# Performance work log

Hardware: AMD Instinct MI355X
Metric: run time of the kernel (lower is better)

Reference implementation:

```python
import jax, jax.numpy as jnp
import numpy as np

B = 8
N_PER = 8192   # xyz points per batch
M_PER = 2048   # query points per batch
C_FEAT = 32
RADIUS = 0.2
K = 32         # sample_nums
USE_XYZ = True


def setup_inputs() -> dict:
    key = jax.random.key(0)
    k1, k2, k3 = jax.random.split(key, 3)
    xyz = jax.random.uniform(k1, (B * N_PER, 3), dtype=jnp.float32)
    new_xyz = jax.random.uniform(k2, (B * M_PER, 3), dtype=jnp.float32)
    features = jax.random.normal(k3, (B * N_PER, C_FEAT), dtype=jnp.float32)
    xyz_batch_cnt = jnp.full((B,), N_PER, dtype=jnp.int32)
    new_xyz_batch_cnt = jnp.full((B,), M_PER, dtype=jnp.int32)
    return {
        "xyz": xyz,
        "xyz_batch_cnt": xyz_batch_cnt,
        "new_xyz": new_xyz,
        "new_xyz_batch_cnt": new_xyz_batch_cnt,
        "features": features,
    }


def _ball_query(xyz_b, new_b, radius, k):
    # xyz_b: (B, N, 3), new_b: (B, M, 3)
    n = xyz_b.shape[1]
    # squared pairwise distances (B, M, N)
    d2 = jnp.sum((new_b[:, :, None, :] - xyz_b[:, None, :, :]) ** 2, axis=-1)
    mask = d2 < (radius * radius)
    # first-k in-radius indices (CUDA ball_query keeps neighbors in point order)
    scores = jnp.where(mask, jnp.arange(n, dtype=jnp.int32), jnp.int32(n))
    idx_sorted = jnp.sort(scores, axis=-1)[..., :k]          # (B, M, k)
    cnt = jnp.sum(mask, axis=-1)                              # (B, M)
    empty = cnt == 0                                          # (B, M)
    first = idx_sorted[..., :1]                               # duplicate first hit
    slot = jnp.arange(k, dtype=jnp.int32)
    idx = jnp.where(slot[None, None, :] < cnt[..., None], idx_sorted, first)
    idx = jnp.where(empty[..., None], jnp.int32(0), idx)      # empty balls -> 0
    return idx, empty


def reference(xyz, xyz_batch_cnt, new_xyz, new_xyz_batch_cnt, features):
    b = xyz_batch_cnt.shape[0]
    xyz_b = xyz.reshape(b, -1, 3)          # (B, N, 3)
    new_b = new_xyz.reshape(b, -1, 3)      # (B, M, 3)
    feat_b = features.reshape(b, xyz_b.shape[1], -1)  # (B, N, C)

    idx, empty = _ball_query(xyz_b, new_b, RADIUS, K)  # (B, M, K), (B, M)

    gather = jax.vmap(lambda pts, i: pts[i])           # per-batch gather
    grouped_xyz = gather(xyz_b, idx) - new_b[:, :, None, :]   # (B, M, K, 3)
    grouped_xyz = jnp.where(empty[..., None, None], 0.0, grouped_xyz)

    grouped_feat = gather(feat_b, idx)                        # (B, M, K, C)
    grouped_feat = jnp.where(empty[..., None, None], 0.0, grouped_feat)

    if USE_XYZ:
        new_features = jnp.concatenate([grouped_xyz, grouped_feat], axis=-1)
    else:
        new_features = grouped_feat
    # (B, M, K, 3+C) -> (B*M, 3+C, K) to match torch (Mtot, C', nsample)
    m_tot = b * new_b.shape[1]
    new_features = jnp.transpose(new_features, (0, 1, 3, 2)).reshape(
        m_tot, -1, K)
    idx_flat = idx.reshape(m_tot, K)
    return new_features, idx_flat
```

## Files before the change

kernel.cpp:

```cpp
#include <hip/hip_runtime.h>

#define BATCHES   8
#define N_PER     8192
#define M_PER     2048
#define C_FEAT    32
#define KNN       32
#define R2        0.04f
#define M_TOT     (BATCHES * M_PER)
#define FEAT_OUT  (3 + C_FEAT)
#define OUT_FEAT_SZ ((size_t)M_TOT * FEAT_OUT * KNN)

__global__ __launch_bounds__(256) void sqag_kernel(
    const float* __restrict__ xyz,
    const float* __restrict__ new_xyz,
    const float* __restrict__ features,
    float* __restrict__ out)
{
    __shared__ int sidx_all[4][2][KNN];

    const int wave       = threadIdx.x >> 6;
    const int lane       = threadIdx.x & 63;
    const int wave_global = blockIdx.x * 4 + wave;

    int cnts[2];

    #pragma unroll
    for (int h = 0; h < 2; ++h) {
        const int q    = wave_global * 2 + h;
        const int b    = q >> 11;
        const int base = b * N_PER;

        const float px = new_xyz[q * 3 + 0];
        const float py = new_xyz[q * 3 + 1];
        const float pz = new_xyz[q * 3 + 2];

        int cnt = 0;
        int first = 0;

        for (int cb = 0; cb < N_PER; cb += 64) {
            const int i = cb + lane;
            const float x = xyz[(size_t)(base + i) * 3 + 0];
            const float y = xyz[(size_t)(base + i) * 3 + 1];
            const float z = xyz[(size_t)(base + i) * 3 + 2];
            const float dx = px - x;
            const float dy = py - y;
            const float dz = pz - z;
            const float d2 = __fadd_rn(__fadd_rn(__fmul_rn(dx, dx),
                                                 __fmul_rn(dy, dy)),
                                       __fmul_rn(dz, dz));
            const bool in = d2 < R2;
            const unsigned long long m = __ballot(in);
            if (m) {
                if (cnt == 0) first = cb + (__ffsll((long long)m) - 1);
                if (in) {
                    const int rank = cnt +
                        __popcll(m & ((1ull << lane) - 1ull));
                    if (rank < KNN) sidx_all[wave][h][rank] = i;
                }
                cnt += __popcll(m);
                if (cnt >= KNN) break;
            }
        }

        const int pad = (cnt == 0) ? 0 : first;
        if (lane >= cnt && lane < KNN) sidx_all[wave][h][lane] = pad;

        cnts[h] = cnt;
    }

    __syncthreads();

    const int h   = lane >> 5;
    const int k   = lane & 31;
    const int q   = wave_global * 2 + h;
    const int b   = q >> 11;
    const int base = b * N_PER;

    const bool empty = (cnts[h] == 0);
    const float zf   = empty ? 0.0f : 1.0f;

    const int li = sidx_all[wave][h][k];
    const int gi = base + li;

    const float px = new_xyz[q * 3 + 0];
    const float py = new_xyz[q * 3 + 1];
    const float pz = new_xyz[q * 3 + 2];

    const float gx = xyz[(size_t)gi * 3 + 0] - px;
    const float gy = xyz[(size_t)gi * 3 + 1] - py;
    const float gz = xyz[(size_t)gi * 3 + 2] - pz;

    float* o = out + (size_t)q * (FEAT_OUT * KNN);
    o[0 * KNN + k] = zf * gx;
    o[1 * KNN + k] = zf * gy;
    o[2 * KNN + k] = zf * gz;

    const float4* f = (const float4*)(features + (size_t)gi * C_FEAT);
    #pragma unroll
    for (int j4 = 0; j4 < C_FEAT / 4; ++j4) {
        const float4 v = f[j4];
        o[(3 + j4 * 4 + 0) * KNN + k] = zf * v.x;
        o[(3 + j4 * 4 + 1) * KNN + k] = zf * v.y;
        o[(3 + j4 * 4 + 2) * KNN + k] = zf * v.z;
        o[(3 + j4 * 4 + 3) * KNN + k] = zf * v.w;
    }

    out[OUT_FEAT_SZ + (size_t)q * KNN + k] = (float)li;
}

extern "C" void kernel_launch(void* const* d_in, const int* in_sizes, int n_in,
                              void* d_out, int out_size, void* d_ws, size_t ws_size,
                              hipStream_t stream) {
    const float* xyz      = (const float*)d_in[0];
    const float* new_xyz  = (const float*)d_in[2];
    const float* features = (const float*)d_in[4];
    float* out = (float*)d_out;

    const int blocks = (M_TOT / 2 + 3) / 4;
    sqag_kernel<<<blocks, 256, 0, stream>>>(xyz, new_xyz, features, out);
}
```

Measured before the change: 133.5 us.

## Split ball query and grouping into two kernels with prefetched scan

Splits the fused kernel into a ball-query kernel that runs one query per wave and a separate grouping kernel with one thread per (query, slot). The scan now covers two 64-point chunks per iteration and software-prefetches the next chunk's coordinates. Empty balls are signalled by writing -0.0 into the index output, which the grouping kernel decodes. This is meant to raise parallelism in the latency-bound scan and shorten each wave's serial work. The cost is an extra launch and an extra round-trip of the indices through global memory.

```diff
diff --git a/kernel.cpp b/kernel.cpp
--- a/kernel.cpp
+++ b/kernel.cpp
@@ -10,77 +10,102 @@
 #define FEAT_OUT  (3 + C_FEAT)
 #define OUT_FEAT_SZ ((size_t)M_TOT * FEAT_OUT * KNN)
 
-__global__ __launch_bounds__(256) void sqag_kernel(
+__global__ __launch_bounds__(256) void ballquery_kernel(
+    const float* __restrict__ xyz,
+    const float* __restrict__ new_xyz,
+    float* __restrict__ out)
+{
+    __shared__ int sidx[4][KNN];
+
+    const int wave = threadIdx.x >> 6;
+    const int lane = threadIdx.x & 63;
+    const int q    = blockIdx.x * 4 + wave;
+    const int b    = q >> 11;
+    const int base = b * N_PER;
+
+    const float px = new_xyz[q * 3 + 0];
+    const float py = new_xyz[q * 3 + 1];
+    const float pz = new_xyz[q * 3 + 2];
+
+    const unsigned long long below = (1ull << lane) - 1ull;
+
+    int cnt = 0;
+    int first = 0;
+
+    const float* p0 = xyz + (size_t)(base + lane) * 3;
+    float x0 = p0[0], y0 = p0[1], z0 = p0[2];
+    float x1 = p0[192], y1 = p0[193], z1 = p0[194];
+
+    for (int cb = 0;;) {
+        const int nb = cb + 128;
+        const bool more = nb < N_PER;
+        float ax0 = 0.f, ay0 = 0.f, az0 = 0.f, ax1 = 0.f, ay1 = 0.f, az1 = 0.f;
+        if (more) {
+            const float* pn = xyz + (size_t)(base + nb + lane) * 3;
+            ax0 = pn[0];   ay0 = pn[1];   az0 = pn[2];
+            ax1 = pn[192]; ay1 = pn[193]; az1 = pn[194];
+        }
+
+        const float dx0 = px - x0, dy0 = py - y0, dz0 = pz - z0;
+        const float dx1 = px - x1, dy1 = py - y1, dz1 = pz - z1;
+        const float d20 = __fadd_rn(__fadd_rn(__fmul_rn(dx0, dx0),
+                                              __fmul_rn(dy0, dy0)),
+                                    __fmul_rn(dz0, dz0));
+        const float d21 = __fadd_rn(__fadd_rn(__fmul_rn(dx1, dx1),
+                                              __fmul_rn(dy1, dy1)),
+                                    __fmul_rn(dz1, dz1));
+        const bool in0 = d20 < R2;
+        const bool in1 = d21 < R2;
+        const unsigned long long m0 = __ballot(in0);
+        const unsigned long long m1 = __ballot(in1);
+
+        if (cnt == 0) {
+            if (m0)      first = cb + (__ffsll((long long)m0) - 1);
+            else if (m1) first = cb + 64 + (__ffsll((long long)m1) - 1);
+        }
+        const int c0 = __popcll(m0);
+        if (in0) {
+            const int r = cnt + __popcll(m0 & below);
+            if (r < KNN) sidx[wave][r] = cb + lane;
+        }
+        if (in1) {
+            const int r = cnt + c0 + __popcll(m1 & below);
+            if (r < KNN) sidx[wave][r] = cb + 64 + lane;
+        }
+        cnt += c0 + __popcll(m1);
+
+        if (cnt >= KNN || !more) break;
+        x0 = ax0; y0 = ay0; z0 = az0;
+        x1 = ax1; y1 = ay1; z1 = az1;
+        cb = nb;
+    }
+
+    const int pad = (cnt == 0) ? 0 : first;
+    if (lane < KNN) {
+        const int li = (lane < cnt) ? sidx[wave][lane] : pad;
+        float f = (float)li;
+        if (cnt == 0) f = -0.0f;
+        out[OUT_FEAT_SZ + (size_t)q * KNN + lane] = f;
+    }
+}
+
+__global__ __launch_bounds__(256) void group_kernel(
     const float* __restrict__ xyz,
     const float* __restrict__ new_xyz,
     const float* __restrict__ features,
     float* __restrict__ out)
 {
-    __shared__ int sidx_all[4][2][KNN];
-
-    const int wave       = threadIdx.x >> 6;
-    const int lane       = threadIdx.x & 63;
-    const int wave_global = blockIdx.x * 4 + wave;
-
-    int cnts[2];
-
-    #pragma unroll
-    for (int h = 0; h < 2; ++h) {
-        const int q    = wave_global * 2 + h;
-        const int b    = q >> 11;
-        const int base = b * N_PER;
-
-        const float px = new_xyz[q * 3 + 0];
-        const float py = new_xyz[q * 3 + 1];
-        const float pz = new_xyz[q * 3 + 2];
-
-        int cnt = 0;
-        int first = 0;
-
-        for (int cb = 0; cb < N_PER; cb += 64) {
-            const int i = cb + lane;
-            const float x = xyz[(size_t)(base + i) * 3 + 0];
-            const float y = xyz[(size_t)(base + i) * 3 + 1];
-            const float z = xyz[(size_t)(base + i) * 3 + 2];
-            const float dx = px - x;
-            const float dy = py - y;
-            const float dz = pz - z;
-            const float d2 = __fadd_rn(__fadd_rn(__fmul_rn(dx, dx),
-                                                 __fmul_rn(dy, dy)),
-                                       __fmul_rn(dz, dz));
-            const bool in = d2 < R2;
-            const unsigned long long m = __ballot(in);
-            if (m) {
-                if (cnt == 0) first = cb + (__ffsll((long long)m) - 1);
-                if (in) {
-                    const int rank = cnt +
-                        __popcll(m & ((1ull << lane) - 1ull));
-                    if (rank < KNN) sidx_all[wave][h][rank] = i;
-                }
-                cnt += __popcll(m);
-                if (cnt >= KNN) break;
-            }
-        }
-
-        const int pad = (cnt == 0) ? 0 : first;
-        if (lane >= cnt && lane < KNN) sidx_all[wave][h][lane] = pad;
-
-        cnts[h] = cnt;
-    }
-
-    __syncthreads();
-
-    const int h   = lane >> 5;
-    const int k   = lane & 31;
-    const int q   = wave_global * 2 + h;
+    const int tid = blockIdx.x * 256 + threadIdx.x;
+    const int q   = tid >> 5;
+    const int k   = tid & 31;
     const int b   = q >> 11;
     const int base = b * N_PER;
 
-    const bool empty = (cnts[h] == 0);
+    const float fidx = out[OUT_FEAT_SZ + (size_t)q * KNN + k];
+    const bool empty = (__float_as_uint(fidx) >> 31) != 0;
     const float zf   = empty ? 0.0f : 1.0f;
-
-    const int li = sidx_all[wave][h][k];
-    const int gi = base + li;
+    const int li     = (int)fidx;
+    const int gi     = base + li;
 
     const float px = new_xyz[q * 3 + 0];
     const float py = new_xyz[q * 3 + 1];
@@ -104,8 +129,6 @@
         o[(3 + j4 * 4 + 2) * KNN + k] = zf * v.z;
         o[(3 + j4 * 4 + 3) * KNN + k] = zf * v.w;
     }
-
-    out[OUT_FEAT_SZ + (size_t)q * KNN + k] = (float)li;
 }
 
 extern "C" void kernel_launch(void* const* d_in, const int* in_sizes, int n_in,
@@ -116,6 +139,6 @@
     const float* features = (const float*)d_in[4];
     float* out = (float*)d_out;
 
-    const int blocks = (M_TOT / 2 + 3) / 4;
-    sqag_kernel<<<blocks, 256, 0, stream>>>(xyz, new_xyz, features, out);
+    ballquery_kernel<<<M_TOT / 4, 256, 0, stream>>>(xyz, new_xyz, out);
+    group_kernel<<<(M_TOT * KNN) / 256, 256, 0, stream>>>(xyz, new_xyz, features, out);
 }
```

Result: no change. 135.7 us (+1.7%).
